# Kernel optimization log

Hardware: AMD Instinct MI355X
Metric: run time of the kernel (lower is better)

## Reference

```python
import jax, jax.numpy as jnp
import numpy as np

# Module hyper-params (from init_kwargs)
M = 41            # filter taps (odd)
OVERLAPS = 40     # even
STRIDES = 216
N_FFT = OVERLAPS + STRIDES   # 256
HOP = STRIDES                # strides > 0 -> hop = strides
PAD = M // 2


def setup_inputs() -> dict:
    key = jax.random.key(0)
    ks = jax.random.split(key, 5)
    B, Nmodes = 2, 2
    steps = 4628
    L = (steps - 1) * HOP + N_FFT  # 999688, frames tile the signal exactly
    x_real = jax.random.normal(ks[0], (B, L, Nmodes), jnp.float32)
    x_imag = jax.random.normal(ks[1], (B, L, Nmodes), jnp.float32)
    task_info = jax.random.uniform(ks[2], (B, 4), jnp.float32)  # col 0 = power (dBm)
    # SnseFilter learned complex taps (shared across polarizations, step=1, n_fwm=0)
    h_real = jax.random.normal(ks[3], (M,), jnp.float32) * 0.01
    h_imag = jax.random.normal(ks[4], (M,), jnp.float32) * 0.01
    return {"x_real": x_real, "x_imag": x_imag, "task_info": task_info,
            "h_real": h_real, "h_imag": h_imag}


def _corr1d(I, h):
    # I: [N, Lp] real, h: [M] real -> valid cross-correlation [N, Lp-M+1]
    out = jax.lax.conv_general_dilated(I[:, None, :], h.reshape(1, 1, M),
                                       window_strides=(1,), padding='VALID')
    return out[:, 0, :]


def reference(x_real, x_imag, task_info, h_real, h_imag):
    x = x_real + 1j * x_imag          # [B, L, Nmodes] complex64
    B, L, Nm = x.shape
    steps = (L - N_FFT) // HOP + 1

    # ---- STFT along dim=1 (frame + FFT, rectangular window, center=False) ----
    idx = HOP * jnp.arange(steps)[:, None] + jnp.arange(N_FFT)[None, :]  # [steps, n_fft]
    frames = x[:, idx, :]                      # [B, steps, n_fft, Nm]
    X = jnp.fft.fft(frames, axis=2)            # frequency-domain frames

    # ---- periodic padding along frequency axis + SnseFilter (per-tap nonlinear PBC) ----
    Xp = jnp.concatenate([X[:, :, -PAD:, :], X, X[:, :, :PAD, :]], axis=2)  # [B,steps,Lp,Nm]
    I = jnp.sum(Xp.real ** 2 + Xp.imag ** 2, axis=-1)   # total intensity over modes [B,steps,Lp]
    Lp = N_FFT + 2 * PAD
    Ic = I.reshape(B * steps, Lp)
    phi = (_corr1d(Ic, h_real) + 1j * _corr1d(Ic, h_imag)).reshape(B, steps, N_FFT)
    # launch power from task_info (col 0 in dBm), per mode
    P = (10.0 ** (task_info[:, 0] / 10.0) / Nm).astype(jnp.float32)  # [B]
    # first-order perturbation: E_out = E + j * P * (h * I) * E  (Manakov diagonal term)
    Y = X * (1.0 + 1j * P[:, None, None, None] * phi[..., None])

    # ---- ISTFT: ifft each frame + overlap-add with rectangular-window normalization ----
    yf = jnp.fft.ifft(Y, axis=2)               # [B, steps, n_fft, Nm]
    flat_idx = idx.reshape(-1)
    ola = jnp.zeros((B, L, Nm), yf.dtype).at[:, flat_idx, :].add(
        yf.reshape(B, steps * N_FFT, Nm))
    wsum = jnp.zeros((L,), jnp.float32).at[flat_idx].add(1.0)  # frame coverage count
    y = ola / wsum[None, :, None]

    out = y[:, OVERLAPS // 2: L - OVERLAPS // 2, :]   # [B, L-overlaps, Nm] complex
    return jnp.stack([out.real, out.imag], axis=-1)    # real view [B, L-overlaps, Nm, 2]
```

## Files before the change

kernel.cpp:

```cpp
#include <hip/hip_runtime.h>
#include <math.h>

constexpr int NFFT = 256;
constexpr int HOP  = 216;
constexpr int PAD  = 20;
constexpr int LPW  = 296;
constexpr int IPS  = 308;

__device__ __forceinline__ void cmul(float& dr, float& di, float ar, float ai, float br, float bi) {
    dr = ar * br - ai * bi;
    di = ar * bi + ai * br;
}

constexpr float TC16[10] = {1.f, 0.92387953f, 0.70710678f, 0.38268343f, 0.f,
                            -0.38268343f, -0.70710678f, -0.92387953f, -1.f, -0.92387953f};
constexpr float TS16[10] = {0.f, 0.38268343f, 0.70710678f, 0.92387953f, 1.f,
                            0.92387953f, 0.70710678f, 0.38268343f, 0.f, -0.38268343f};

template<int SGN>
__device__ __forceinline__ void fft16(float xr[16], float xi[16]) {
    constexpr float S = (float)SGN;
    float tr[4][4], ti[4][4];
    #pragma unroll
    for (int n1 = 0; n1 < 4; ++n1) {
        float ar = xr[n1],      ai = xi[n1];
        float br = xr[n1 + 4],  bi = xi[n1 + 4];
        float cr = xr[n1 + 8],  ci = xi[n1 + 8];
        float dr = xr[n1 + 12], di = xi[n1 + 12];
        float Ar = ar + cr, Ai = ai + ci, Br = ar - cr, Bi = ai - ci;
        float Cr = br + dr, Ci = bi + di, Dr = br - dr, Di = bi - di;
        tr[n1][0] = Ar + Cr;      ti[n1][0] = Ai + Ci;
        tr[n1][2] = Ar - Cr;      ti[n1][2] = Ai - Ci;
        tr[n1][1] = Br - S * Di;  ti[n1][1] = Bi + S * Dr;
        tr[n1][3] = Br + S * Di;  ti[n1][3] = Bi - S * Dr;
    }
    #pragma unroll
    for (int n1 = 1; n1 < 4; ++n1) {
        #pragma unroll
        for (int k2 = 1; k2 < 4; ++k2) {
            const int m = n1 * k2;
            const float wr = TC16[m], wi = S * TS16[m];
            float vr, vi;
            cmul(vr, vi, tr[n1][k2], ti[n1][k2], wr, wi);
            tr[n1][k2] = vr; ti[n1][k2] = vi;
        }
    }
    #pragma unroll
    for (int k2 = 0; k2 < 4; ++k2) {
        float ar = tr[0][k2], ai = ti[0][k2];
        float br = tr[1][k2], bi = ti[1][k2];
        float cr = tr[2][k2], ci = ti[2][k2];
        float dr = tr[3][k2], di = ti[3][k2];
        float Ar = ar + cr, Ai = ai + ci, Br = ar - cr, Bi = ai - ci;
        float Cr = br + dr, Ci = bi + di, Dr = br - dr, Di = bi - di;
        xr[k2]      = Ar + Cr;     xi[k2]      = Ai + Ci;
        xr[k2 + 8]  = Ar - Cr;     xi[k2 + 8]  = Ai - Ci;
        xr[k2 + 4]  = Br - S * Di; xi[k2 + 4]  = Bi + S * Dr;
        xr[k2 + 12] = Br + S * Di; xi[k2 + 12] = Bi - S * Dr;
    }
}

__global__ __launch_bounds__(128)
void zero_overlap(float* __restrict__ out, int B, int steps, int Lout) {
    const int s = blockIdx.x + 1;
    const int total = B * 160;
    for (int j = threadIdx.x; j < total; j += 128) {
        const int bb = j / 160;
        const int r  = j - bb * 160;
        out[((size_t)bb * Lout + (size_t)s * HOP - PAD) * 4 + r] = 0.0f;
    }
}

__global__ __launch_bounds__(256)
void eq_pbc_kernel(const float* __restrict__ x_real,
                   const float* __restrict__ x_imag,
                   const float* __restrict__ task_info,
                   const float* __restrict__ h_real,
                   const float* __restrict__ h_imag,
                   float* __restrict__ out,
                   int B, int L, int steps)
{
    __shared__ __align__(16) float SM[8704];

    const int tid = threadIdx.x;
    const int i   = tid & 15;
    const int fm  = tid >> 4;
    const int fr  = tid >> 5;
    const int md  = fm & 1;
    const int u   = tid & 31;

    const int G = B * steps;
    int g = blockIdx.x * 8 + fr;
    const bool valid = (g < G);
    if (!valid) g = G - 1;
    const int b  = g / steps;
    const int s  = g - b * steps;
    const int l0 = s * HOP;

    float sb, cb;
    __sincosf(-6.2831853071795864f * (1.0f / 256.0f) * (float)i, &sb, &cb);

    float xr[16], xi[16];
    {
        const size_t base = ((size_t)b * L + l0) * 2 + (size_t)(2 * i + md);
        #pragma unroll
        for (int n2 = 0; n2 < 16; ++n2) {
            xr[n2] = x_real[base + 32 * n2];
            xi[n2] = x_imag[base + 32 * n2];
        }
    }

    fft16<-1>(xr, xi);

    {
        float wr[16], wi[16];
        wr[1] = cb; wi[1] = sb;
        #pragma unroll
        for (int k = 2; k < 16; ++k) {
            const int h = k >> 1;
            cmul(wr[k], wi[k], wr[h], wi[h], wr[k - h], wi[k - h]);
        }
        #pragma unroll
        for (int k = 1; k < 16; ++k) {
            float vr, vi;
            cmul(vr, vi, xr[k], xi[k], wr[k], wi[k]);
            xr[k] = vr; xi[k] = vi;
        }
    }

    const int tb = fm * 272;
    #pragma unroll
    for (int k = 0; k < 16; ++k) {
        SM[tb + i * 17 + k]        = xr[k];
        SM[4352 + tb + i * 17 + k] = xi[k];
    }
    __syncthreads();
    #pragma unroll
    for (int n1 = 0; n1 < 16; ++n1) {
        xr[n1] = SM[tb + n1 * 17 + i];
        xi[n1] = SM[4352 + tb + n1 * 17 + i];
    }

    fft16<-1>(xr, xi);
    __syncthreads();

    #pragma unroll
    for (int k1 = 0; k1 < 16; ++k1)
        SM[fr * 512 + md * 256 + i + 16 * k1] = xr[k1] * xr[k1] + xi[k1] * xi[k1];
    __syncthreads();

    #pragma unroll
    for (int c = 0; c < 10; ++c) {
        const int p = u + 32 * c;
        if (p < LPW) {
            const int f = (p + 236) & 255;
            SM[4352 + fr * IPS + p] = SM[fr * 512 + f] + SM[fr * 512 + 256 + f];
        }
    }
    __syncthreads();

    {
        float W[48];
        #pragma unroll
        for (int c = 0; c < 12; ++c)
            *(float4*)&W[4 * c] = *(const float4*)&SM[4352 + fr * IPS + u * 8 + 4 * c];
        float phr[8], phi8[8];
        #pragma unroll
        for (int o = 0; o < 8; ++o) { phr[o] = 0.f; phi8[o] = 0.f; }
        #pragma unroll
        for (int t = 0; t < 41; ++t) {
            const float htr = h_real[t], hti = h_imag[t];
            #pragma unroll
            for (int o = 0; o < 8; ++o) {
                phr[o]  = fmaf(W[o + t], htr, phr[o]);
                phi8[o] = fmaf(W[o + t], hti, phi8[o]);
            }
        }
        const float P = exp2f(task_info[4 * b] * 0.33219280948873623f) * 0.5f;
        float4 cr0, cr1, ci0, ci1;
        cr0.x = 1.f - P * phi8[0]; cr0.y = 1.f - P * phi8[1]; cr0.z = 1.f - P * phi8[2]; cr0.w = 1.f - P * phi8[3];
        cr1.x = 1.f - P * phi8[4]; cr1.y = 1.f - P * phi8[5]; cr1.z = 1.f - P * phi8[6]; cr1.w = 1.f - P * phi8[7];
        ci0.x = P * phr[0]; ci0.y = P * phr[1]; ci0.z = P * phr[2]; ci0.w = P * phr[3];
        ci1.x = P * phr[4]; ci1.y = P * phr[5]; ci1.z = P * phr[6]; ci1.w = P * phr[7];
        *(float4*)&SM[fr * 256 + u * 8]          = cr0;
        *(float4*)&SM[fr * 256 + u * 8 + 4]      = cr1;
        *(float4*)&SM[2048 + fr * 256 + u * 8]     = ci0;
        *(float4*)&SM[2048 + fr * 256 + u * 8 + 4] = ci1;
    }
    __syncthreads();

    #pragma unroll
    for (int k1 = 0; k1 < 16; ++k1) {
        const float cr_ = SM[fr * 256 + i + 16 * k1];
        const float ci_ = SM[2048 + fr * 256 + i + 16 * k1];
        const float vr = xr[k1] * cr_ - xi[k1] * ci_;
        const float vi = xr[k1] * ci_ + xi[k1] * cr_;
        xr[k1] = vr; xi[k1] = vi;
    }

    fft16<1>(xr, xi);
    {
        float wr[16], wi[16];
        wr[1] = cb; wi[1] = -sb;
        #pragma unroll
        for (int k = 2; k < 16; ++k) {
            const int h = k >> 1;
            cmul(wr[k], wi[k], wr[h], wi[h], wr[k - h], wi[k - h]);
        }
        #pragma unroll
        for (int k = 1; k < 16; ++k) {
            float vr, vi;
            cmul(vr, vi, xr[k], xi[k], wr[k], wi[k]);
            xr[k] = vr; xi[k] = vi;
        }
    }
    __syncthreads();

    #pragma unroll
    for (int k = 0; k < 16; ++k) {
        SM[tb + i * 17 + k]        = xr[k];
        SM[4352 + tb + i * 17 + k] = xi[k];
    }
    __syncthreads();
    #pragma unroll
    for (int k2 = 0; k2 < 16; ++k2) {
        xr[k2] = SM[tb + k2 * 17 + i];
        xi[k2] = SM[4352 + tb + k2 * 17 + i];
    }

    fft16<1>(xr, xi);

    if (valid) {
        const int Lout = L - 2 * PAD;
        float* obase = out + (size_t)b * Lout * 4 + md * 2;
        #pragma unroll
        for (int n2 = 0; n2 < 16; ++n2) {
            const int n  = i + 16 * n2;
            const int la = l0 + n;
            if (la < PAD || la >= L - PAD) continue;
            const bool ov = (n < NFFT - HOP && s > 0) || (n >= HOP && s + 1 < steps);
            const float sc = (ov ? 0.5f : 1.0f) * (1.0f / 256.0f);
            float* p = obase + (size_t)(la - PAD) * 4;
            const float vr = xr[n2] * sc, vi = xi[n2] * sc;
            if (ov) { atomicAdd(p, vr); atomicAdd(p + 1, vi); }
            else    { *(float2*)p = make_float2(vr, vi); }
        }
    }
}

extern "C" void kernel_launch(void* const* d_in, const int* in_sizes, int n_in,
                              void* d_out, int out_size, void* d_ws, size_t ws_size,
                              hipStream_t stream) {
    const float* x_real    = (const float*)d_in[0];
    const float* x_imag    = (const float*)d_in[1];
    const float* task_info = (const float*)d_in[2];
    const float* h_real    = (const float*)d_in[3];
    const float* h_imag    = (const float*)d_in[4];

    const int B     = in_sizes[2] / 4;
    const int L     = in_sizes[0] / (B * 2);
    const int steps = (L - NFFT) / HOP + 1;
    const int G     = B * steps;
    const int Lout  = L - 2 * PAD;

    if (steps > 1)
        zero_overlap<<<steps - 1, 128, 0, stream>>>((float*)d_out, B, steps, Lout);

    eq_pbc_kernel<<<(G + 7) / 8, 256, 0, stream>>>(
        x_real, x_imag, task_info, h_real, h_imag, (float*)d_out, B, L, steps);
}
```

Baseline: 118.7 us.

## Shrink blocks to four frames, cut shared memory, and vectorize zeroing kernel

The main kernel now processes four frames per 128-thread block and uses a smaller shared-memory footprint. It transposes real and imaginary parts in sequence through one float4-written buffer, and builds the periodic-padded intensity with shared atomics into a pre-zeroed buffer instead of a separate gather pass. The overlap-zeroing kernel becomes a grid-stride loop writing float4s. The aim is higher occupancy and fewer shared-memory passes, at the cost of extra barriers and LDS atomics.

```diff
diff --git a/kernel.cpp b/kernel.cpp
--- a/kernel.cpp
+++ b/kernel.cpp
@@ -4,8 +4,13 @@
 constexpr int NFFT = 256;
 constexpr int HOP  = 216;
 constexpr int PAD  = 20;
-constexpr int LPW  = 296;
-constexpr int IPS  = 308;
+
+constexpr int TRS = 20;
+constexpr int TPS = 328;
+constexpr int TSZ = 8 * TPS;
+constexpr int IPS = 312;
+constexpr int IP0 = TSZ;
+constexpr int SMF = TSZ + 4 * IPS;
 
 __device__ __forceinline__ void cmul(float& dr, float& di, float ar, float ai, float br, float bi) {
     dr = ar * br - ai * bi;
@@ -60,18 +65,19 @@
     }
 }
 
+__global__ __launch_bounds__(256)
+void zero_overlap(float4* __restrict__ out4, int B, int steps, int Lout) {
+    const int total = B * (steps - 1) * 40;
+    for (int idx = blockIdx.x * 256 + threadIdx.x; idx < total; idx += gridDim.x * 256) {
+        const int j  = idx / 40;
+        const int r4 = idx - j * 40;
+        const int b  = j / (steps - 1);
+        const int s  = j - b * (steps - 1) + 1;
+        out4[(size_t)b * Lout + (size_t)s * HOP - PAD + r4] = make_float4(0.f, 0.f, 0.f, 0.f);
+    }
+}
+
 __global__ __launch_bounds__(128)
-void zero_overlap(float* __restrict__ out, int B, int steps, int Lout) {
-    const int s = blockIdx.x + 1;
-    const int total = B * 160;
-    for (int j = threadIdx.x; j < total; j += 128) {
-        const int bb = j / 160;
-        const int r  = j - bb * 160;
-        out[((size_t)bb * Lout + (size_t)s * HOP - PAD) * 4 + r] = 0.0f;
-    }
-}
-
-__global__ __launch_bounds__(256)
 void eq_pbc_kernel(const float* __restrict__ x_real,
                    const float* __restrict__ x_imag,
                    const float* __restrict__ task_info,
@@ -80,23 +86,27 @@
                    float* __restrict__ out,
                    int B, int L, int steps)
 {
-    __shared__ __align__(16) float SM[8704];
+    __shared__ __align__(16) float SM[SMF];
 
     const int tid = threadIdx.x;
     const int i   = tid & 15;
     const int fm  = tid >> 4;
     const int fr  = tid >> 5;
-    const int md  = fm & 1;
+    const int md  = (tid >> 4) & 1;
     const int u   = tid & 31;
 
     const int G = B * steps;
-    int g = blockIdx.x * 8 + fr;
+    int g = blockIdx.x * 4 + fr;
     const bool valid = (g < G);
     if (!valid) g = G - 1;
     const int b  = g / steps;
     const int s  = g - b * steps;
     const int l0 = s * HOP;
 
+    #pragma unroll
+    for (int j = tid; j < 4 * IPS / 4; j += 128)
+        *(float4*)&SM[IP0 + 4 * j] = make_float4(0.f, 0.f, 0.f, 0.f);
+
     float sb, cb;
     __sincosf(-6.2831853071795864f * (1.0f / 256.0f) * (float)i, &sb, &cb);
 
@@ -111,7 +121,6 @@
     }
 
     fft16<-1>(xr, xi);
-
     {
         float wr[16], wi[16];
         wr[1] = cb; wi[1] = sb;
@@ -128,33 +137,32 @@
         }
     }
 
-    const int tb = fm * 272;
-    #pragma unroll
-    for (int k = 0; k < 16; ++k) {
-        SM[tb + i * 17 + k]        = xr[k];
-        SM[4352 + tb + i * 17 + k] = xi[k];
-    }
-    __syncthreads();
-    #pragma unroll
-    for (int n1 = 0; n1 < 16; ++n1) {
-        xr[n1] = SM[tb + n1 * 17 + i];
-        xi[n1] = SM[4352 + tb + n1 * 17 + i];
-    }
+    const int tb = fm * TPS;
+    #pragma unroll
+    for (int c = 0; c < 4; ++c)
+        *(float4*)&SM[tb + i * TRS + 4 * c] = make_float4(xr[4*c], xr[4*c+1], xr[4*c+2], xr[4*c+3]);
+    __syncthreads();
+    #pragma unroll
+    for (int n1 = 0; n1 < 16; ++n1) xr[n1] = SM[tb + n1 * TRS + i];
+    __syncthreads();
+    #pragma unroll
+    for (int c = 0; c < 4; ++c)
+        *(float4*)&SM[tb + i * TRS + 4 * c] = make_float4(xi[4*c], xi[4*c+1], xi[4*c+2], xi[4*c+3]);
+    __syncthreads();
+    #pragma unroll
+    for (int n1 = 0; n1 < 16; ++n1) xi[n1] = SM[tb + n1 * TRS + i];
 
     fft16<-1>(xr, xi);
-    __syncthreads();
-
-    #pragma unroll
-    for (int k1 = 0; k1 < 16; ++k1)
-        SM[fr * 512 + md * 256 + i + 16 * k1] = xr[k1] * xr[k1] + xi[k1] * xi[k1];
-    __syncthreads();
-
-    #pragma unroll
-    for (int c = 0; c < 10; ++c) {
-        const int p = u + 32 * c;
-        if (p < LPW) {
-            const int f = (p + 236) & 255;
-            SM[4352 + fr * IPS + p] = SM[fr * 512 + f] + SM[fr * 512 + 256 + f];
+
+    {
+        float* ip = &SM[IP0 + fr * IPS];
+        #pragma unroll
+        for (int k1 = 0; k1 < 16; ++k1) {
+            const int f = i + 16 * k1;
+            const float v = xr[k1] * xr[k1] + xi[k1] * xi[k1];
+            atomicAdd(&ip[f + PAD], v);
+            if (f < PAD)         atomicAdd(&ip[f + 276], v);
+            if (f >= NFFT - PAD) atomicAdd(&ip[f - 236], v);
         }
     }
     __syncthreads();
@@ -163,7 +171,7 @@
         float W[48];
         #pragma unroll
         for (int c = 0; c < 12; ++c)
-            *(float4*)&W[4 * c] = *(const float4*)&SM[4352 + fr * IPS + u * 8 + 4 * c];
+            *(float4*)&W[4 * c] = *(const float4*)&SM[IP0 + fr * IPS + u * 8 + 4 * c];
         float phr[8], phi8[8];
         #pragma unroll
         for (int o = 0; o < 8; ++o) { phr[o] = 0.f; phi8[o] = 0.f; }
@@ -177,22 +185,22 @@
             }
         }
         const float P = exp2f(task_info[4 * b] * 0.33219280948873623f) * 0.5f;
-        float4 cr0, cr1, ci0, ci1;
-        cr0.x = 1.f - P * phi8[0]; cr0.y = 1.f - P * phi8[1]; cr0.z = 1.f - P * phi8[2]; cr0.w = 1.f - P * phi8[3];
-        cr1.x = 1.f - P * phi8[4]; cr1.y = 1.f - P * phi8[5]; cr1.z = 1.f - P * phi8[6]; cr1.w = 1.f - P * phi8[7];
-        ci0.x = P * phr[0]; ci0.y = P * phr[1]; ci0.z = P * phr[2]; ci0.w = P * phr[3];
-        ci1.x = P * phr[4]; ci1.y = P * phr[5]; ci1.z = P * phr[6]; ci1.w = P * phr[7];
-        *(float4*)&SM[fr * 256 + u * 8]          = cr0;
-        *(float4*)&SM[fr * 256 + u * 8 + 4]      = cr1;
-        *(float4*)&SM[2048 + fr * 256 + u * 8]     = ci0;
-        *(float4*)&SM[2048 + fr * 256 + u * 8 + 4] = ci1;
+        float4 v0, v1;
+        v0.x = 1.f - P * phi8[0]; v0.y = 1.f - P * phi8[1]; v0.z = 1.f - P * phi8[2]; v0.w = 1.f - P * phi8[3];
+        v1.x = 1.f - P * phi8[4]; v1.y = 1.f - P * phi8[5]; v1.z = 1.f - P * phi8[6]; v1.w = 1.f - P * phi8[7];
+        *(float4*)&SM[fr * 512 + u * 8]     = v0;
+        *(float4*)&SM[fr * 512 + u * 8 + 4] = v1;
+        v0.x = P * phr[0]; v0.y = P * phr[1]; v0.z = P * phr[2]; v0.w = P * phr[3];
+        v1.x = P * phr[4]; v1.y = P * phr[5]; v1.z = P * phr[6]; v1.w = P * phr[7];
+        *(float4*)&SM[fr * 512 + 256 + u * 8]     = v0;
+        *(float4*)&SM[fr * 512 + 256 + u * 8 + 4] = v1;
     }
     __syncthreads();
 
     #pragma unroll
     for (int k1 = 0; k1 < 16; ++k1) {
-        const float cr_ = SM[fr * 256 + i + 16 * k1];
-        const float ci_ = SM[2048 + fr * 256 + i + 16 * k1];
+        const float cr_ = SM[fr * 512 + i + 16 * k1];
+        const float ci_ = SM[fr * 512 + 256 + i + 16 * k1];
         const float vr = xr[k1] * cr_ - xi[k1] * ci_;
         const float vi = xr[k1] * ci_ + xi[k1] * cr_;
         xr[k1] = vr; xi[k1] = vi;
@@ -217,16 +225,18 @@
     __syncthreads();
 
     #pragma unroll
-    for (int k = 0; k < 16; ++k) {
-        SM[tb + i * 17 + k]        = xr[k];
-        SM[4352 + tb + i * 17 + k] = xi[k];
-    }
-    __syncthreads();
-    #pragma unroll
-    for (int k2 = 0; k2 < 16; ++k2) {
-        xr[k2] = SM[tb + k2 * 17 + i];
-        xi[k2] = SM[4352 + tb + k2 * 17 + i];
-    }
+    for (int c = 0; c < 4; ++c)
+        *(float4*)&SM[tb + i * TRS + 4 * c] = make_float4(xr[4*c], xr[4*c+1], xr[4*c+2], xr[4*c+3]);
+    __syncthreads();
+    #pragma unroll
+    for (int k2 = 0; k2 < 16; ++k2) xr[k2] = SM[tb + k2 * TRS + i];
+    __syncthreads();
+    #pragma unroll
+    for (int c = 0; c < 4; ++c)
+        *(float4*)&SM[tb + i * TRS + 4 * c] = make_float4(xi[4*c], xi[4*c+1], xi[4*c+2], xi[4*c+3]);
+    __syncthreads();
+    #pragma unroll
+    for (int k2 = 0; k2 < 16; ++k2) xi[k2] = SM[tb + k2 * TRS + i];
 
     fft16<1>(xr, xi);
 
@@ -263,9 +273,12 @@
     const int G     = B * steps;
     const int Lout  = L - 2 * PAD;
 
-    if (steps > 1)
-        zero_overlap<<<steps - 1, 128, 0, stream>>>((float*)d_out, B, steps, Lout);
-
-    eq_pbc_kernel<<<(G + 7) / 8, 256, 0, stream>>>(
+    if (steps > 1) {
+        const int total4 = B * (steps - 1) * 40;
+        const int zb = (total4 + 255) / 256;
+        zero_overlap<<<zb, 256, 0, stream>>>((float4*)d_out, B, steps, Lout);
+    }
+
+    eq_pbc_kernel<<<(G + 3) / 4, 128, 0, stream>>>(
         x_real, x_imag, task_info, h_real, h_imag, (float*)d_out, B, L, steps);
 }
```

Measured after the change: 136.1 us. 1.15x slower.
